# Optimization experiments

Measured on AMD Instinct MI355X. Metric: run time of the kernel, lower is better.

The kernel has to match this reference:

```python
import jax, jax.numpy as jnp
import numpy as np

IN_DIM = 64
OUT_DIM = 64
SPLINE_ORDER = 3
GRID_SIZE = 8
GRID_LOW, GRID_HIGH = -1.0, 1.0
BATCH = 2048


def generate_control_points(low, high, in_dim, out_dim, spline_order, grid_size):
    # Knot vector extended spline_order points beyond the range on each side.
    spacing = (high - low) / grid_size
    knots = jnp.arange(-spline_order, grid_size + spline_order + 1, dtype=jnp.float32) * spacing + low
    # (out_dim, in_dim, grid_size + 2*spline_order + 1)
    return jnp.broadcast_to(knots, (out_dim, in_dim, knots.shape[0]))


def compute_bspline(x, grid, k):
    """Cox-de Boor recursion.
    x:    (B, in_dim)
    grid: (out_dim, in_dim, G + 2k + 1)
    returns bases: (B, out_dim, in_dim, G + k)
    """
    xe = x[:, None, :, None]  # (B, 1, in, 1)
    g = grid[None]            # (1, out, in, n_knots)
    bases = ((xe >= g[..., :-1]) & (xe < g[..., 1:])).astype(x.dtype)
    for j in range(1, k + 1):
        left = (xe - g[..., : -(j + 1)]) / (g[..., j:-1] - g[..., : -(j + 1)])
        right = (g[..., j + 1 :] - xe) / (g[..., j + 1 :] - g[..., 1:-j])
        bases = left * bases[..., :-1] + right * bases[..., 1:]
    return bases


def setup_inputs() -> dict:
    key = jax.random.key(0)
    kx, kc = jax.random.split(key)
    x = jax.random.normal(kx, (BATCH, IN_DIM), dtype=jnp.float32)
    grid = generate_control_points(GRID_LOW, GRID_HIGH, IN_DIM, OUT_DIM, SPLINE_ORDER, GRID_SIZE)
    # xavier_normal_ on (out, in, G+k): fan_in = in*(G+k), fan_out = out*(G+k)
    n_coef = GRID_SIZE + SPLINE_ORDER
    std = float(np.sqrt(2.0 / (IN_DIM * n_coef + OUT_DIM * n_coef)))
    coef = jax.random.normal(kc, (OUT_DIM, IN_DIM, n_coef), dtype=jnp.float32) * std
    return {"x": x, "grid": grid, "coef": coef}


def reference(x, grid, coef):
    bases = compute_bspline(x, grid, SPLINE_ORDER)        # (B, out, in, G+k)
    spline = jnp.sum(bases * coef[None], axis=-1)          # (B, out, in)
    return spline
```

## Files before the change

kernel.cpp:

```cpp
#include <hip/hip_runtime.h>


#define BATCH    2048
#define IN_DIM   64
#define OUT_DIM  64
#define NCOEF    11
#define B_TILE   4
#define O_TILE   16
#define NPAIR    (B_TILE * IN_DIM)
#define PLANE    (NPAIR * 4)

__global__ __launch_bounds__(256) void kan_kernel(
    const float* __restrict__ x,
    const float* __restrict__ grid,
    const float* __restrict__ coef,
    float* __restrict__ out)
{
    __shared__ float lds[3 * PLANE];

    const int tid    = threadIdx.x;
    const int o_tile = blockIdx.x & 3;
    const int b_tile = blockIdx.x >> 2;
    const int b0     = b_tile * B_TILE;

    const float g0    = grid[0];
    const float inv_h = 1.0f / (grid[1] - g0);

    {
        const int p  = tid;
        const int bb = p >> 6;
        const int i  = p & 63;
        const float xv = x[(size_t)(b0 + bb) * IN_DIM + i];

        const float4 z = make_float4(0.f, 0.f, 0.f, 0.f);
        *(float4*)&lds[0 * PLANE + p * 4] = z;
        *(float4*)&lds[1 * PLANE + p * 4] = z;
        *(float4*)&lds[2 * PLANE + p * 4] = z;

        const float pos = (xv - g0) * inv_h;
        if (pos >= 0.0f && pos < 14.0f) {
            const int   m  = (int)pos;
            const float t  = pos - (float)m;
            const float t2 = t * t;
            const float t3 = t2 * t;
            const float s  = 1.0f - t;
            const float w0 = s * s * s * (1.0f / 6.0f);
            const float w1 = (3.0f * t3 - 6.0f * t2 + 4.0f) * (1.0f / 6.0f);
            const float w2 = (-3.0f * t3 + 3.0f * t2 + 3.0f * t + 1.0f) * (1.0f / 6.0f);
            const float w3 = t3 * (1.0f / 6.0f);

            const int mb = m - 3;
            int idx;
            idx = mb + 0; if ((unsigned)idx < NCOEF) lds[(idx >> 2) * PLANE + p * 4 + (idx & 3)] = w0;
            idx = mb + 1; if ((unsigned)idx < NCOEF) lds[(idx >> 2) * PLANE + p * 4 + (idx & 3)] = w1;
            idx = mb + 2; if ((unsigned)idx < NCOEF) lds[(idx >> 2) * PLANE + p * 4 + (idx & 3)] = w2;
            idx = mb + 3; if ((unsigned)idx < NCOEF) lds[(idx >> 2) * PLANE + p * 4 + (idx & 3)] = w3;
        }
    }
    __syncthreads();

    const int i   = tid & 63;
    const int grp = tid >> 6;
    const int o   = o_tile * O_TILE + grp * 4;

    float c[4][NCOEF];
    const float* cp = &coef[((size_t)o * IN_DIM + i) * NCOEF];
    #pragma unroll
    for (int oo = 0; oo < 4; ++oo)
        #pragma unroll
        for (int t = 0; t < NCOEF; ++t)
            c[oo][t] = cp[(size_t)oo * IN_DIM * NCOEF + t];

    #pragma unroll
    for (int bb = 0; bb < B_TILE; ++bb) {
        const int p = bb * IN_DIM + i;
        const float4 v0 = *(const float4*)&lds[0 * PLANE + p * 4];
        const float4 v1 = *(const float4*)&lds[1 * PLANE + p * 4];
        const float4 v2 = *(const float4*)&lds[2 * PLANE + p * 4];

        float* op = &out[(size_t)(b0 + bb) * (OUT_DIM * IN_DIM) + o * IN_DIM + i];
        #pragma unroll
        for (int oo = 0; oo < 4; ++oo) {
            float acc;
            acc  = v0.x * c[oo][0] + v0.y * c[oo][1] + v0.z * c[oo][2] + v0.w * c[oo][3];
            acc += v1.x * c[oo][4] + v1.y * c[oo][5] + v1.z * c[oo][6] + v1.w * c[oo][7];
            acc += v2.x * c[oo][8] + v2.y * c[oo][9] + v2.z * c[oo][10];
            __builtin_nontemporal_store(acc, op + oo * IN_DIM);
        }
    }
}

extern "C" void kernel_launch(void* const* d_in, const int* in_sizes, int n_in,
                              void* d_out, int out_size, void* d_ws, size_t ws_size,
                              hipStream_t stream) {
    const float* x    = (const float*)d_in[0];
    const float* grid = (const float*)d_in[1];
    const float* coef = (const float*)d_in[2];
    float* out = (float*)d_out;

    const int nblocks = (BATCH / B_TILE) * (OUT_DIM / O_TILE);
    kan_kernel<<<nblocks, 256, 0, stream>>>(x, grid, coef, out);
}
```

Before: 16.54 us.

## Stage coef tile in LDS and compute basis weights per thread in registers

The kernel now cooperatively loads each block's 16-output coefficient slice into LDS with coalesced reads, then each thread pulls its coefficients from LDS instead of strided global loads. Basis weights are no longer staged in LDS: each thread recomputes the cubic B-spline weights for its input column per batch row, building a dense 11-wide vector with selects. The batch chunk per block doubles to 8, halving the grid, and output stores drop the nontemporal hint. This trades LDS traffic and a barrier-separated phase for redundant per-thread weight arithmetic and select chains, plus a 45 KB LDS footprint that may limit occupancy.

```diff
diff --git a/kernel.cpp b/kernel.cpp
--- a/kernel.cpp
+++ b/kernel.cpp
@@ -5,10 +5,9 @@
 #define IN_DIM   64
 #define OUT_DIM  64
 #define NCOEF    11
-#define B_TILE   4
-#define O_TILE   16
-#define NPAIR    (B_TILE * IN_DIM)
-#define PLANE    (NPAIR * 4)
+#define B_CHUNK  8
+#define O_BLK    16
+#define CTILE    (O_BLK * IN_DIM * NCOEF)
 
 __global__ __launch_bounds__(256) void kan_kernel(
     const float* __restrict__ x,
@@ -16,76 +15,68 @@
     const float* __restrict__ coef,
     float* __restrict__ out)
 {
-    __shared__ float lds[3 * PLANE];
+    __shared__ float clds[CTILE];
 
     const int tid    = threadIdx.x;
     const int o_tile = blockIdx.x & 3;
-    const int b_tile = blockIdx.x >> 2;
-    const int b0     = b_tile * B_TILE;
+    const int b0     = (blockIdx.x >> 2) * B_CHUNK;
+
+    const float* csrc = coef + (size_t)o_tile * CTILE;
+    #pragma unroll
+    for (int q = 0; q < CTILE / 256; ++q)
+        clds[tid + q * 256] = csrc[tid + q * 256];
 
     const float g0    = grid[0];
     const float inv_h = 1.0f / (grid[1] - g0);
 
-    {
-        const int p  = tid;
-        const int bb = p >> 6;
-        const int i  = p & 63;
-        const float xv = x[(size_t)(b0 + bb) * IN_DIM + i];
-
-        const float4 z = make_float4(0.f, 0.f, 0.f, 0.f);
-        *(float4*)&lds[0 * PLANE + p * 4] = z;
-        *(float4*)&lds[1 * PLANE + p * 4] = z;
-        *(float4*)&lds[2 * PLANE + p * 4] = z;
-
-        const float pos = (xv - g0) * inv_h;
-        if (pos >= 0.0f && pos < 14.0f) {
-            const int   m  = (int)pos;
-            const float t  = pos - (float)m;
-            const float t2 = t * t;
-            const float t3 = t2 * t;
-            const float s  = 1.0f - t;
-            const float w0 = s * s * s * (1.0f / 6.0f);
-            const float w1 = (3.0f * t3 - 6.0f * t2 + 4.0f) * (1.0f / 6.0f);
-            const float w2 = (-3.0f * t3 + 3.0f * t2 + 3.0f * t + 1.0f) * (1.0f / 6.0f);
-            const float w3 = t3 * (1.0f / 6.0f);
-
-            const int mb = m - 3;
-            int idx;
-            idx = mb + 0; if ((unsigned)idx < NCOEF) lds[(idx >> 2) * PLANE + p * 4 + (idx & 3)] = w0;
-            idx = mb + 1; if ((unsigned)idx < NCOEF) lds[(idx >> 2) * PLANE + p * 4 + (idx & 3)] = w1;
-            idx = mb + 2; if ((unsigned)idx < NCOEF) lds[(idx >> 2) * PLANE + p * 4 + (idx & 3)] = w2;
-            idx = mb + 3; if ((unsigned)idx < NCOEF) lds[(idx >> 2) * PLANE + p * 4 + (idx & 3)] = w3;
-        }
-    }
     __syncthreads();
 
-    const int i   = tid & 63;
-    const int grp = tid >> 6;
-    const int o   = o_tile * O_TILE + grp * 4;
+    const int i    = tid & 63;
+    const int ogrp = tid >> 6;
+    const int ol0  = ogrp * 4;
+    const int o0   = o_tile * O_BLK + ol0;
 
     float c[4][NCOEF];
-    const float* cp = &coef[((size_t)o * IN_DIM + i) * NCOEF];
     #pragma unroll
-    for (int oo = 0; oo < 4; ++oo)
+    for (int oo = 0; oo < 4; ++oo) {
+        const int row = ((ol0 + oo) * IN_DIM + i) * NCOEF;
         #pragma unroll
         for (int t = 0; t < NCOEF; ++t)
-            c[oo][t] = cp[(size_t)oo * IN_DIM * NCOEF + t];
+            c[oo][t] = clds[row + t];
+    }
 
-    #pragma unroll
-    for (int bb = 0; bb < B_TILE; ++bb) {
-        const int p = bb * IN_DIM + i;
-        const float4 v0 = *(const float4*)&lds[0 * PLANE + p * 4];
-        const float4 v1 = *(const float4*)&lds[1 * PLANE + p * 4];
-        const float4 v2 = *(const float4*)&lds[2 * PLANE + p * 4];
+    #pragma unroll 2
+    for (int bb = 0; bb < B_CHUNK; ++bb) {
+        const float xv  = x[(size_t)(b0 + bb) * IN_DIM + i];
+        const float pos = (xv - g0) * inv_h;
+        const float fm  = floorf(pos);
+        const float t   = pos - fm;
+        const int   base = (pos >= 0.0f && pos < 14.0f) ? ((int)fm - 3) : -1000;
 
-        float* op = &out[(size_t)(b0 + bb) * (OUT_DIM * IN_DIM) + o * IN_DIM + i];
+        const float t2 = t * t;
+        const float t3 = t2 * t;
+        const float s  = 1.0f - t;
+        const float w0 = s * s * s * (1.0f / 6.0f);
+        const float w1 = (3.0f * t3 - 6.0f * t2 + 4.0f) * (1.0f / 6.0f);
+        const float w2 = (-3.0f * t3 + 3.0f * t2 + 3.0f * t + 1.0f) * (1.0f / 6.0f);
+        const float w3 = t3 * (1.0f / 6.0f);
+
+        float dense[NCOEF];
+        #pragma unroll
+        for (int tt = 0; tt < NCOEF; ++tt) {
+            const int d = tt - base;
+            dense[tt] = (d == 0) ? w0 : (d == 1) ? w1 : (d == 2) ? w2
+                      : (d == 3) ? w3 : 0.0f;
+        }
+
+        float* op = &out[(size_t)(b0 + bb) * (OUT_DIM * IN_DIM) + o0 * IN_DIM + i];
         #pragma unroll
         for (int oo = 0; oo < 4; ++oo) {
-            float acc;
-            acc  = v0.x * c[oo][0] + v0.y * c[oo][1] + v0.z * c[oo][2] + v0.w * c[oo][3];
-            acc += v1.x * c[oo][4] + v1.y * c[oo][5] + v1.z * c[oo][6] + v1.w * c[oo][7];
-            acc += v2.x * c[oo][8] + v2.y * c[oo][9] + v2.z * c[oo][10];
-            __builtin_nontemporal_store(acc, op + oo * IN_DIM);
+            float acc = dense[0] * c[oo][0];
+            #pragma unroll
+            for (int tt = 1; tt < NCOEF; ++tt)
+                acc += dense[tt] * c[oo][tt];
+            op[oo * IN_DIM] = acc;
         }
     }
 }
@@ -98,6 +89,6 @@
     const float* coef = (const float*)d_in[2];
     float* out = (float*)d_out;
 
-    const int nblocks = (BATCH / B_TILE) * (OUT_DIM / O_TILE);
+    const int nblocks = (BATCH / B_CHUNK) * (OUT_DIM / O_BLK);
     kan_kernel<<<nblocks, 256, 0, stream>>>(x, grid, coef, out);
 }
```

Result: slower. 18.95 us (median of 2 runs) (+14.6%).
